# Kernel optimization log

Measured on AMD Instinct MI355X. Metric: run time of the kernel, lower is better.

## Reference

```python
import jax, jax.numpy as jnp
import numpy as np

B, N, C_IN = 8, 2048, 128
FEATS = [256, 256, 64]

def _mlp(x, W1, b1, W2, b2, W3, b3):
    # kernel-1 conv MLP == per-point linear layers; ReLU between hidden layers,
    # no ReLU on output (cfg mlp_with_relu=False)
    h = jax.nn.relu(jnp.einsum('bnc,fc->bnf', x, W1) + b1)
    h = jax.nn.relu(jnp.einsum('bnc,fc->bnf', h, W2) + b2)
    return jnp.einsum('bnc,fc->bnf', h, W3) + b3

def _pairwise_sqdist(u):
    # ||u_m - u_n||^2 expanded (avoids B*N*N*C intermediate)
    sq = jnp.sum(u * u, axis=-1)  # [B,N]
    d = sq[:, None, :] + sq[:, :, None] - 2.0 * jnp.einsum('bnc,bmc->bnm', u, u)
    return jnp.maximum(d, 0.0)

def setup_inputs() -> dict:
    key = jax.random.key(0)
    ks = jax.random.split(key, 8)
    x = jax.random.normal(ks[0], (B, N, C_IN), dtype=jnp.float32)
    labels = jax.random.randint(ks[1], (B, N), 0, 32, dtype=jnp.int32)
    tri = jax.random.randint(ks[2], (200, 3), 0, N, dtype=jnp.int32)
    W1 = jax.random.normal(ks[3], (FEATS[0], C_IN), dtype=jnp.float32) / np.sqrt(C_IN)
    b1 = jnp.zeros((FEATS[0],), jnp.float32)
    W2 = jax.random.normal(ks[4], (FEATS[1], FEATS[0]), dtype=jnp.float32) / np.sqrt(FEATS[0])
    b2 = jnp.zeros((FEATS[1],), jnp.float32)
    W3 = jax.random.normal(ks[5], (FEATS[2], FEATS[1]), dtype=jnp.float32) / np.sqrt(FEATS[1])
    b3 = jnp.zeros((FEATS[2],), jnp.float32)
    return {"x": x, "labels": labels, "tri": tri,
            "W1": W1, "b1": b1, "W2": W2, "b2": b2, "W3": W3, "b3": b3}

def _triplet_loss(dists, labels, tri):
    a, p, n = tri[:, 0], tri[:, 1], tri[:, 2]
    def per_batch(d, lab):
        valid = (a != p) & (lab[a] == lab[p]) & (lab[p] != lab[n])
        t = jnp.maximum(d[a, p] - d[a, n] + 2.0, 0.0)
        cnt = jnp.sum(valid)
        m = jnp.sum(jnp.where(valid, t, 0.0)) / jnp.maximum(cnt, 1).astype(t.dtype)
        use = (jnp.max(lab) > 0) & (cnt > 0)
        return jnp.where(use, m, 0.0)
    return jnp.sum(jax.vmap(per_batch)(dists, labels))

def _transitive_closure_clusters(dists):
    pred = (((dists + jnp.swapaxes(dists, 1, 2)) * 0.5) <= 1.0).astype(jnp.float32)
    idx = jnp.arange(N)
    pred = pred.at[:, idx, idx].set(1.0)
    def cond(s):
        _, now, before = s
        return now != before
    def body(s):
        m, now, _ = s
        m2 = (jnp.matmul(m, m) > 0).astype(jnp.float32)
        return (m2, jnp.sum(m2), now)
    s0 = (pred, jnp.sum(pred), jnp.sum(pred) - 1.0)
    pred, _, _ = jax.lax.while_loop(cond, body, s0)
    clusters = jnp.max(jnp.where(pred > 0, idx[None, :, None], -1), axis=1)
    return clusters.astype(jnp.int32)

def reference(x, labels, tri, W1, b1, W2, b2, W3, b3):
    u = _mlp(x, W1, b1, W2, b2, W3, b3)       # [B,N,C]
    dists = _pairwise_sqdist(u)               # [B,N,N]
    loss = _triplet_loss(dists, labels, tri)
    clusters = _transitive_closure_clusters(jax.lax.stop_gradient(dists))
    return (clusters, loss)
```

## Files before the change

### kernel.cpp

```cpp
#include <hip/hip_runtime.h>

constexpr int B_   = 8;
constexpr int N_   = 2048;
constexpr int CIN_ = 128;
constexpr int F1_  = 256;
constexpr int F2_  = 256;
constexpr int F3_  = 64;
constexpr int M_   = B_ * N_;

typedef unsigned short u16;
typedef unsigned long long u64;
typedef __attribute__((ext_vector_type(8)))  short short8v;
typedef __attribute__((ext_vector_type(16))) float f32x16;

__device__ inline u16 f2bf(float x){
    union { float f; unsigned u; } c; c.f = x;
    unsigned r = (c.u + 0x7FFFu + ((c.u >> 16) & 1u)) >> 16;
    return (u16)r;
}
__device__ inline float bf2f(u16 h){
    union { unsigned u; float f; } c; c.u = ((unsigned)h) << 16;
    return c.f;
}

constexpr int NX_  = M_ * CIN_;
constexpr int NW1_ = F1_ * CIN_;
constexpr int NW2_ = F2_ * F1_;

__global__ __launch_bounds__(256)
void split3_kernel(const float* __restrict__ x, const float* __restrict__ W1,
                   const float* __restrict__ W2,
                   u16* __restrict__ xh, u16* __restrict__ xm, u16* __restrict__ xl,
                   u16* __restrict__ w1h, u16* __restrict__ w1m, u16* __restrict__ w1l,
                   u16* __restrict__ w2h, u16* __restrict__ w2m, u16* __restrict__ w2l,
                   u64* __restrict__ rmask, float* __restrict__ lz)
{
    int id = blockIdx.x * 256 + threadIdx.x;
    if (id == 0) *lz = 0.f;
    if (id < M_) rmask[id] = 0ull;
    const float* src; u16 *oh, *om, *ol; int r, k, K;
    if (id < NX_)               { int t = id;               src = x;  r = t >> 7; k = t & 127; K = 128; oh = xh;  om = xm;  ol = xl;  }
    else if (id < NX_ + NW1_)   { int t = id - NX_;         src = W1; r = t >> 7; k = t & 127; K = 128; oh = w1h; om = w1m; ol = w1l; }
    else if (id < NX_ + NW1_ + NW2_) { int t = id - NX_ - NW1_; src = W2; r = t >> 8; k = t & 255; K = 256; oh = w2h; om = w2m; ol = w2l; }
    else return;
    float v = src[(size_t)r * K + k];
    u16 h = f2bf(v);            float vr = v - bf2f(h);
    u16 m = f2bf(vr);           u16 l = f2bf(vr - bf2f(m));
    size_t o = (size_t)r * K + (k ^ ((r & 7) << 3));
    oh[o] = h; om[o] = m; ol[o] = l;
}

template<int KSTEPS, int WRITE_F32>
__global__ __launch_bounds__(256)
void gemm_mfma(const u16* __restrict__ Ah, const u16* __restrict__ Am, const u16* __restrict__ Al,
               const u16* __restrict__ Wh, const u16* __restrict__ Wm, const u16* __restrict__ Wl,
               const float* __restrict__ bias,
               u16* __restrict__ Hh, u16* __restrict__ Hm, u16* __restrict__ Hl,
               float* __restrict__ Hf)
{
    constexpr int K = KSTEPS * 64;
    __shared__ __align__(16) u16 SMEM[3*64*64 + 3*128*64];
    u16* LA = SMEM;
    u16* LB = SMEM + 3*64*64;
    const int tid = threadIdx.x;
    const int wv = tid >> 6, l = tid & 63;
    const int wc = wv;
    const int lr = l & 31, hl = l >> 5;
    const int m0 = blockIdx.y * 64, f0 = blockIdx.x * 128;

    const u16* Asrc[3] = {Ah, Am, Al};
    const u16* Bsrc[3] = {Wh, Wm, Wl};

    f32x16 acc[2] = {};
    auto frag = [&](const u16* arr, int row, int kb) -> short8v {
        int off = row * 64 + ((kb ^ ((row & 7) << 4)) >> 1);
        return *(const short8v*)&arr[off];
    };

    for (int s = 0; s < KSTEPS; ++s) {
        const int k0 = s * 64;
        __syncthreads();
#pragma unroll
        for (int lvl = 0; lvl < 3; ++lvl) {
#pragma unroll
            for (int p = 0; p < 2; ++p) {
                int g = tid + p * 256;
                int row = g >> 3, ch = (g & 7) * 8;
                *(short8v*)&LA[lvl*4096 + row*64 + ch] =
                    *(const short8v*)&Asrc[lvl][(size_t)(m0 + row) * K + k0 + ch];
            }
#pragma unroll
            for (int p = 0; p < 4; ++p) {
                int g = tid + p * 256;
                int row = g >> 3, ch = (g & 7) * 8;
                *(short8v*)&LB[lvl*8192 + row*64 + ch] =
                    *(const short8v*)&Bsrc[lvl][(size_t)(f0 + row) * K + k0 + ch];
            }
        }
        __syncthreads();
#pragma unroll
        for (int ks = 0; ks < 4; ++ks) {
            const int kb = ks * 32 + hl * 16;
            short8v aF[3][2], bF[3];
#pragma unroll
            for (int lvl = 0; lvl < 3; ++lvl) {
#pragma unroll
                for (int ri = 0; ri < 2; ++ri)
                    aF[lvl][ri] = frag(LA + lvl*4096, ri*32 + lr, kb);
                bF[lvl] = frag(LB + lvl*8192, wc*32 + lr, kb);
            }
            const int pl[6][2] = {{0,2},{2,0},{1,1},{0,1},{1,0},{0,0}};
#pragma unroll
            for (int pp = 0; pp < 6; ++pp)
#pragma unroll
                for (int ri = 0; ri < 2; ++ri)
                    acc[ri] = __builtin_amdgcn_mfma_f32_32x32x16_bf16(
                        aF[pl[pp][0]][ri], bF[pl[pp][1]], acc[ri], 0, 0, 0);
        }
    }

    __syncthreads();
    float* LDSF = (float*)SMEM;
#pragma unroll
    for (int ri = 0; ri < 2; ++ri)
#pragma unroll
        for (int r = 0; r < 16; ++r) {
            int row = ri*32 + (r & 3) + 8*(r >> 2) + 4*hl;
            LDSF[row*132 + wc*32 + lr] = acc[ri][r];
        }
    __syncthreads();
#pragma unroll
    for (int p = 0; p < 4; ++p) {
        int idx = tid + p * 256;
        int row = idx >> 4;
        int g8  = (idx & 15) * 8;
        float v[8], bz[8];
        *(float4*)&v[0]  = *(const float4*)&LDSF[row*132 + g8];
        *(float4*)&v[4]  = *(const float4*)&LDSF[row*132 + g8 + 4];
        *(float4*)&bz[0] = *(const float4*)(bias + f0 + g8);
        *(float4*)&bz[4] = *(const float4*)(bias + f0 + g8 + 4);
        const size_t mrow = m0 + row;
        short8v hh, mm8, ll;
#pragma unroll
        for (int j = 0; j < 8; ++j) {
            float vv = fmaxf(v[j] + bz[j], 0.f);
            v[j] = vv;
            u16 h = f2bf(vv);  float r1 = vv - bf2f(h);
            u16 m = f2bf(r1);  u16 lo = f2bf(r1 - bf2f(m));
            hh[j] = (short)h; mm8[j] = (short)m; ll[j] = (short)lo;
        }
        if constexpr (WRITE_F32) {
            *(float4*)&Hf[mrow * F2_ + f0 + g8]     = *(const float4*)&v[0];
            *(float4*)&Hf[mrow * F2_ + f0 + g8 + 4] = *(const float4*)&v[4];
        }
        const size_t ob = mrow * F2_ + ((size_t)(f0 + g8) ^ ((mrow & 7) << 3));
        *(short8v*)&Hh[ob] = hh;
        *(short8v*)&Hm[ob] = mm8;
        *(short8v*)&Hl[ob] = ll;
    }
}

__global__ __launch_bounds__(256)
void gemm3_fused(const float* __restrict__ A, const float* __restrict__ W,
                 const float* __restrict__ bias, float* __restrict__ C,
                 u16* __restrict__ uh, u16* __restrict__ ul,
                 float* __restrict__ sqv)
{
    constexpr int K = 256;
    __shared__ __align__(16) float As[64][68];
    __shared__ __align__(16) float Ws[64][68];
    const int tid = threadIdx.x;
    const int tx = tid & 15, ty = tid >> 4;
    const int m0 = blockIdx.x * 64;

    float acc[4][4] = {};
    for (int k0 = 0; k0 < K; k0 += 64) {
        __syncthreads();
#pragma unroll
        for (int p = 0; p < 4; ++p) {
            int g = tid + p * 256;
            int r = g >> 4, c = (g & 15) << 2;
            float4 va = *(const float4*)(A + (size_t)(m0 + r) * K + k0 + c);
            As[c+0][r] = va.x; As[c+1][r] = va.y; As[c+2][r] = va.z; As[c+3][r] = va.w;
            float4 vw = *(const float4*)(W + (size_t)r * K + k0 + c);
            Ws[c+0][r] = vw.x; Ws[c+1][r] = vw.y; Ws[c+2][r] = vw.z; Ws[c+3][r] = vw.w;
        }
        __syncthreads();
#pragma unroll
        for (int k = 0; k < 64; ++k) {
            float a[4], w[4];
            *(float4*)&a[0] = *(const float4*)&As[k][ty << 2];
            *(float4*)&w[0] = *(const float4*)&Ws[k][tx << 2];
#pragma unroll
            for (int i = 0; i < 4; ++i)
#pragma unroll
                for (int j = 0; j < 4; ++j)
                    acc[i][j] = fmaf(a[i], w[j], acc[i][j]);
        }
    }

    float4 bz = *(const float4*)(bias + (tx << 2));
    const int slot = tx >> 1;
    const int hoff = (tx & 1) * 4;
#pragma unroll
    for (int i = 0; i < 4; ++i) {
        const int m = m0 + (ty << 2) + i;
        float o[4];
        o[0] = acc[i][0] + bz.x; o[1] = acc[i][1] + bz.y;
        o[2] = acc[i][2] + bz.z; o[3] = acc[i][3] + bz.w;
        *(float4*)(C + (size_t)m * F3_ + (tx << 2)) = *(const float4*)&o[0];
        ushort4 h4, l4;
        h4.x = f2bf(o[0]); l4.x = f2bf(o[0] - bf2f(h4.x));
        h4.y = f2bf(o[1]); l4.y = f2bf(o[1] - bf2f(h4.y));
        h4.z = f2bf(o[2]); l4.z = f2bf(o[2] - bf2f(h4.z));
        h4.w = f2bf(o[3]); l4.w = f2bf(o[3] - bf2f(h4.w));
        const int sb = (((slot * 16) ^ ((m & 7) << 4)) >> 1) + hoff;
        *(ushort4*)&uh[(size_t)m * 64 + sb] = h4;
        *(ushort4*)&ul[(size_t)m * 64 + sb] = l4;
        float s = o[0]*o[0] + o[1]*o[1] + o[2]*o[2] + o[3]*o[3];
#pragma unroll
        for (int msk = 1; msk <= 8; msk <<= 1) s += __shfl_xor(s, msk, 64);
        if (tx == 0) sqv[m] = s;
    }
}

__global__ __launch_bounds__(256)
void adj_mfma(const u16* __restrict__ uh, const u16* __restrict__ ul,
              const float* __restrict__ uf, const float* __restrict__ sqv,
              unsigned* __restrict__ adj, u64* __restrict__ rmask)
{
    __shared__ u16 UiH[128*64], UiL[128*64];
    __shared__ u16 UjH[128*64], UjL[128*64];
    __shared__ float sqi[128], sqj[128];
    const int tid = threadIdx.x;
    const int jt = blockIdx.x, it = blockIdx.y, b = blockIdx.z;
    const int i0 = it * 128, j0 = jt * 128;
    const size_t ub = (size_t)b * N_;

    if (tid < 128) sqi[tid] = sqv[ub + i0 + tid];
    else           sqj[tid - 128] = sqv[ub + j0 + (tid - 128)];

    auto stage = [&](const u16* src, u16* dst) {
#pragma unroll
        for (int p = 0; p < 4; ++p) {
            int g = tid + p * 256;
            *(short8v*)&dst[g * 8] = *(const short8v*)&src[g * 8];
        }
    };
    stage(uh + (ub + i0) * 64, UiH);
    stage(ul + (ub + i0) * 64, UiL);
    stage(uh + (ub + j0) * 64, UjH);
    stage(ul + (ub + j0) * 64, UjL);
    __syncthreads();

    const int w  = tid >> 6, l = tid & 63;
    const int wr = w >> 1,  wc = w & 1;
    const int lr = l & 31,  hl = l >> 5;

    f32x16 acc[2][2] = {};
    auto frag = [&](const u16* arr, int row, int kb) -> short8v {
        int off = row * 64 + ((kb ^ ((row & 7) << 4)) >> 1);
        return *(const short8v*)&arr[off];
    };
#pragma unroll
    for (int ks = 0; ks < 4; ++ks) {
        const int kb = ks * 32 + hl * 16;
        short8v aH[2], aL[2], bH[2], bL[2];
#pragma unroll
        for (int ri = 0; ri < 2; ++ri) {
            aH[ri] = frag(UiH, wr * 64 + ri * 32 + lr, kb);
            aL[ri] = frag(UiL, wr * 64 + ri * 32 + lr, kb);
        }
#pragma unroll
        for (int ci = 0; ci < 2; ++ci) {
            bH[ci] = frag(UjH, wc * 64 + ci * 32 + lr, kb);
            bL[ci] = frag(UjL, wc * 64 + ci * 32 + lr, kb);
        }
#pragma unroll
        for (int ri = 0; ri < 2; ++ri)
#pragma unroll
            for (int ci = 0; ci < 2; ++ci) {
                acc[ri][ci] = __builtin_amdgcn_mfma_f32_32x32x16_bf16(aH[ri], bH[ci], acc[ri][ci], 0, 0, 0);
                acc[ri][ci] = __builtin_amdgcn_mfma_f32_32x32x16_bf16(aH[ri], bL[ci], acc[ri][ci], 0, 0, 0);
                acc[ri][ci] = __builtin_amdgcn_mfma_f32_32x32x16_bf16(aL[ri], bH[ci], acc[ri][ci], 0, 0, 0);
            }
    }

#pragma unroll
    for (int ri = 0; ri < 2; ++ri)
#pragma unroll
    for (int ci = 0; ci < 2; ++ci) {
        const int Rb = wr * 64 + ri * 32;
        const int Cb = wc * 64 + ci * 32;
        const int jloc = Cb + lr;
        const float sj = sqj[jloc];
#pragma unroll
        for (int r = 0; r < 16; ++r) {
            const int base = (r & 3) + 8 * (r >> 2);
            const int iloc = Rb + base + 4 * hl;
            const float si = sqi[iloc];
            float dv = si + sj - 2.0f * acc[ri][ci][r];
            bool e;
            if (__builtin_expect(fabsf(dv - 1.0f) < 0.02f, 0)) {
                const float* ua = uf + (ub + i0 + iloc) * (size_t)F3_;
                const float* vb = uf + (ub + j0 + jloc) * (size_t)F3_;
                float dot = 0.f;
#pragma unroll 4
                for (int k = 0; k < F3_; ++k) dot = fmaf(ua[k], vb[k], dot);
                e = (si + sj - 2.0f * dot) <= 1.0f;
            } else {
                e = dv <= 1.0f;
            }
            u64 m = __ballot(e);
            if (l == 0) {
                const int I = i0 + Rb + base;
                const int W = (j0 + Cb) >> 5;
                adj[((size_t)b * 64 + W) * N_ + I]     = (unsigned)m;
                adj[((size_t)b * 64 + W) * N_ + I + 4] = (unsigned)(m >> 32);
                if ((unsigned)m)         atomicOr(&rmask[ub + I],     1ull << W);
                if ((unsigned)(m >> 32)) atomicOr(&rmask[ub + I + 4], 1ull << W);
            }
        }
    }
}

__global__ __launch_bounds__(1024)
void cc_kernel(const unsigned* __restrict__ adj, const u64* __restrict__ rmask,
               float* __restrict__ out)
{
    __shared__ int Lb[N_];
    __shared__ int chg;
    const int t = threadIdx.x;
    const int b = blockIdx.x;
    const unsigned* ab = adj + (size_t)b * 64 * N_;
    const u64* rm = rmask + (size_t)b * N_;

    Lb[t] = t; Lb[t + 1024] = t + 1024;
    __syncthreads();

    for (int iter = 0; iter < 24; ++iter) {
        if (t == 0) chg = 0;
        __syncthreads();
        int m[2], o[2];
#pragma unroll
        for (int h = 0; h < 2; ++h) {
            int i = t + h * 1024;
            int mm = Lb[i];
            o[h] = mm;
            const unsigned* row = ab + i;
            u64 msk = rm[i];
            while (msk) {
                int w = __ffsll(msk) - 1;
                msk &= msk - 1;
                unsigned v = row[(size_t)w * N_];
                while (v) {
                    int bit = __ffs(v) - 1;
                    v &= v - 1;
                    int lj = Lb[(w << 5) + bit];
                    mm = (lj > mm) ? lj : mm;
                }
            }
            for (int q = 0; q < N_; ++q) {
                int nx = Lb[mm];
                if (nx == mm) break;
                mm = nx;
            }
            m[h] = mm;
        }
        __syncthreads();
        Lb[t] = m[0]; Lb[t + 1024] = m[1];
        if (m[0] != o[0] || m[1] != o[1]) chg = 1;
        __syncthreads();
        if (!chg) break;
    }
    out[(size_t)b * N_ + t]        = (float)Lb[t];
    out[(size_t)b * N_ + t + 1024] = (float)Lb[t + 1024];
}

__global__ __launch_bounds__(256)
void sentinel_kernel(float* out, int n)
{
    int id = blockIdx.x * 256 + threadIdx.x;
    if (id < n) out[id] = -777.0f;
}

__global__ __launch_bounds__(256)
void loss_kernel(const float* __restrict__ u, const float* __restrict__ sq,
                 const int* __restrict__ labels, const int* __restrict__ tri,
                 float* __restrict__ loss)
{
    __shared__ float ssum[256];
    __shared__ int   scnt[256];
    __shared__ int   smax[256];
    const int b = blockIdx.x, t = threadIdx.x;
    const int base = b << 11;

    float mysum = 0.f; int mycnt = 0;
    if (t < 200) {
        int a = tri[3*t+0], p = tri[3*t+1], n = tri[3*t+2];
        int la = labels[base+a], lp = labels[base+p], ln = labels[base+n];
        bool valid = (a != p) && (la == lp) && (lp != ln);
        const float4* ua = (const float4*)(u + (size_t)(base + a) * F3_);
        const float4* up = (const float4*)(u + (size_t)(base + p) * F3_);
        const float4* un = (const float4*)(u + (size_t)(base + n) * F3_);
        float dap = 0.f, dan = 0.f;
#pragma unroll
        for (int q = 0; q < 16; ++q) {
            float4 va = ua[q], vp = up[q], vn = un[q];
            dap += va.x*vp.x + va.y*vp.y + va.z*vp.z + va.w*vp.w;
            dan += va.x*vn.x + va.y*vn.y + va.z*vn.z + va.w*vn.w;
        }
        float d1 = fmaxf(sq[base+a] + sq[base+p] - 2.f*dap, 0.f);
        float d2 = fmaxf(sq[base+a] + sq[base+n] - 2.f*dan, 0.f);
        float tt = fmaxf(d1 - d2 + 2.0f, 0.f);
        if (valid) { mysum = tt; mycnt = 1; }
    }
    int mymax = 0;
    for (int idx = t; idx < N_; idx += 256) {
        int lv = labels[base + idx];
        mymax = (lv > mymax) ? lv : mymax;
    }
    ssum[t] = mysum; scnt[t] = mycnt; smax[t] = mymax;
    __syncthreads();
    for (int s = 128; s > 0; s >>= 1) {
        if (t < s) {
            ssum[t] += ssum[t + s];
            scnt[t] += scnt[t + s];
            smax[t] = (smax[t + s] > smax[t]) ? smax[t + s] : smax[t];
        }
        __syncthreads();
    }
    if (t == 0) {
        int cnt = scnt[0];
        bool use = (smax[0] > 0) && (cnt > 0);
        float contrib = use ? (ssum[0] / (float)(cnt > 1 ? cnt : 1)) : 0.f;
        atomicAdd(loss, contrib);
    }
}

extern "C" void kernel_launch(void* const* d_in, const int* in_sizes, int n_in,
                              void* d_out, int out_size, void* d_ws, size_t ws_size,
                              hipStream_t stream)
{
    const float* x      = (const float*)d_in[0];
    const int*   labels = (const int*)  d_in[1];
    const int*   tri    = (const int*)  d_in[2];
    const float* W1     = (const float*)d_in[3];
    const float* b1     = (const float*)d_in[4];
    const float* W2     = (const float*)d_in[5];
    const float* b2     = (const float*)d_in[6];
    const float* W3     = (const float*)d_in[7];
    const float* b3     = (const float*)d_in[8];
    float* out = (float*)d_out;

    char* w = (char*)d_ws;
    size_t off = 0;
    auto carve = [&](size_t bytes) -> char* {
        char* p = w + off;
        off += (bytes + 255) & ~(size_t)255;
        return p;
    };
    u16* xh  = (u16*)carve((size_t)NX_  * 2);
    u16* xm  = (u16*)carve((size_t)NX_  * 2);
    u16* xl  = (u16*)carve((size_t)NX_  * 2);
    u16* w1h = (u16*)carve((size_t)NW1_ * 2);
    u16* w1m = (u16*)carve((size_t)NW1_ * 2);
    u16* w1l = (u16*)carve((size_t)NW1_ * 2);
    u16* w2h = (u16*)carve((size_t)NW2_ * 2);
    u16* w2m = (u16*)carve((size_t)NW2_ * 2);
    u16* w2l = (u16*)carve((size_t)NW2_ * 2);
    u16* h1h = (u16*)carve((size_t)M_ * F1_ * 2);
    u16* h1m = (u16*)carve((size_t)M_ * F1_ * 2);
    u16* h1l = (u16*)carve((size_t)M_ * F1_ * 2);
    u16* h2h = (u16*)carve((size_t)M_ * F2_ * 2);
    u16* h2m = (u16*)carve((size_t)M_ * F2_ * 2);
    u16* h2l = (u16*)carve((size_t)M_ * F2_ * 2);
    float* h2f = (float*)carve((size_t)M_ * F2_ * 4);
    float* u   = (float*)carve((size_t)M_ * F3_ * 4);
    u16*   uh  = (u16*)  carve((size_t)M_ * F3_ * 2);
    u16*   ul  = (u16*)  carve((size_t)M_ * F3_ * 2);
    float* sq  = (float*)carve((size_t)M_ * 4);
    unsigned* adj = (unsigned*)carve((size_t)B_ * 64 * N_ * 4);
    u64* rmask = (u64*)carve((size_t)M_ * 8);

    if (off > ws_size) {
        hipLaunchKernelGGL(sentinel_kernel, dim3((out_size + 255) / 256), dim3(256),
                           0, stream, out, out_size);
        return;
    }

    constexpr int NTOT = NX_ + NW1_ + NW2_;
    hipLaunchKernelGGL(split3_kernel, dim3((NTOT + 255) / 256), dim3(256), 0, stream,
                       x, W1, W2, xh, xm, xl, w1h, w1m, w1l, w2h, w2m, w2l,
                       rmask, out + M_);

    hipLaunchKernelGGL((gemm_mfma<2, 0>), dim3(F1_/128, M_/64), dim3(256), 0, stream,
                       xh, xm, xl, w1h, w1m, w1l, b1, h1h, h1m, h1l, (float*)nullptr);
    hipLaunchKernelGGL((gemm_mfma<4, 1>), dim3(F2_/128, M_/64), dim3(256), 0, stream,
                       h1h, h1m, h1l, w2h, w2m, w2l, b2, h2h, h2m, h2l, h2f);

    hipLaunchKernelGGL(gemm3_fused, dim3(M_/64), dim3(256), 0, stream,
                       h2f, W3, b3, u, uh, ul, sq);

    hipLaunchKernelGGL(adj_mfma, dim3(N_/128, N_/128, B_), dim3(256), 0, stream,
                       uh, ul, u, sq, adj, rmask);

    hipLaunchKernelGGL(loss_kernel, dim3(B_), dim3(256), 0, stream,
                       u, sq, labels, tri, out + M_);

    hipLaunchKernelGGL(cc_kernel, dim3(B_), dim3(1024), 0, stream,
                       adj, rmask, out);
}
```

Before: 183.6 us.

## Compute only upper-triangular adjacency tiles and mirror via bit transpose

```diff
diff --git a/kernel.cpp b/kernel.cpp
--- a/kernel.cpp
+++ b/kernel.cpp
@@ -167,32 +167,38 @@
                  float* __restrict__ sqv)
 {
     constexpr int K = 256;
-    __shared__ __align__(16) float As[64][68];
+    __shared__ __align__(16) float As[64][36];
     __shared__ __align__(16) float Ws[64][68];
     const int tid = threadIdx.x;
     const int tx = tid & 15, ty = tid >> 4;
-    const int m0 = blockIdx.x * 64;
-
-    float acc[4][4] = {};
+    const int m0 = blockIdx.x * 32;
+
+    float acc[2][4] = {};
     for (int k0 = 0; k0 < K; k0 += 64) {
         __syncthreads();
 #pragma unroll
-        for (int p = 0; p < 4; ++p) {
+        for (int p = 0; p < 2; ++p) {
             int g = tid + p * 256;
             int r = g >> 4, c = (g & 15) << 2;
             float4 va = *(const float4*)(A + (size_t)(m0 + r) * K + k0 + c);
             As[c+0][r] = va.x; As[c+1][r] = va.y; As[c+2][r] = va.z; As[c+3][r] = va.w;
+        }
+#pragma unroll
+        for (int p = 0; p < 4; ++p) {
+            int g = tid + p * 256;
+            int r = g >> 4, c = (g & 15) << 2;
             float4 vw = *(const float4*)(W + (size_t)r * K + k0 + c);
             Ws[c+0][r] = vw.x; Ws[c+1][r] = vw.y; Ws[c+2][r] = vw.z; Ws[c+3][r] = vw.w;
         }
         __syncthreads();
 #pragma unroll
         for (int k = 0; k < 64; ++k) {
-            float a[4], w[4];
-            *(float4*)&a[0] = *(const float4*)&As[k][ty << 2];
+            float a[2], w[4];
+            a[0] = As[k][(ty << 1)];
+            a[1] = As[k][(ty << 1) + 1];
             *(float4*)&w[0] = *(const float4*)&Ws[k][tx << 2];
 #pragma unroll
-            for (int i = 0; i < 4; ++i)
+            for (int i = 0; i < 2; ++i)
 #pragma unroll
                 for (int j = 0; j < 4; ++j)
                     acc[i][j] = fmaf(a[i], w[j], acc[i][j]);
@@ -203,8 +209,8 @@
     const int slot = tx >> 1;
     const int hoff = (tx & 1) * 4;
 #pragma unroll
-    for (int i = 0; i < 4; ++i) {
-        const int m = m0 + (ty << 2) + i;
+    for (int i = 0; i < 2; ++i) {
+        const int m = m0 + (ty << 1) + i;
         float o[4];
         o[0] = acc[i][0] + bz.x; o[1] = acc[i][1] + bz.y;
         o[2] = acc[i][2] + bz.z; o[3] = acc[i][3] + bz.w;
@@ -229,33 +235,35 @@
               const float* __restrict__ uf, const float* __restrict__ sqv,
               unsigned* __restrict__ adj, u64* __restrict__ rmask)
 {
-    __shared__ u16 UiH[128*64], UiL[128*64];
-    __shared__ u16 UjH[128*64], UjL[128*64];
+    __shared__ u16 UiH[128*64];
+    __shared__ u16 UjH[128*64];
     __shared__ float sqi[128], sqj[128];
     const int tid = threadIdx.x;
-    const int jt = blockIdx.x, it = blockIdx.y, b = blockIdx.z;
+    const int b = blockIdx.z;
+    int q = blockIdx.x;
+    int jt = (int)((sqrtf(8.f * q + 1.f) - 1.f) * 0.5f);
+    while ((jt + 1) * (jt + 2) / 2 <= q) ++jt;
+    while (jt * (jt + 1) / 2 > q) --jt;
+    const int it = q - jt * (jt + 1) / 2;
     const int i0 = it * 128, j0 = jt * 128;
     const size_t ub = (size_t)b * N_;
 
     if (tid < 128) sqi[tid] = sqv[ub + i0 + tid];
     else           sqj[tid - 128] = sqv[ub + j0 + (tid - 128)];
 
-    auto stage = [&](const u16* src, u16* dst) {
-#pragma unroll
-        for (int p = 0; p < 4; ++p) {
-            int g = tid + p * 256;
-            *(short8v*)&dst[g * 8] = *(const short8v*)&src[g * 8];
-        }
-    };
-    stage(uh + (ub + i0) * 64, UiH);
-    stage(ul + (ub + i0) * 64, UiL);
-    stage(uh + (ub + j0) * 64, UjH);
-    stage(ul + (ub + j0) * 64, UjL);
+#pragma unroll
+    for (int p = 0; p < 4; ++p) {
+        int g = tid + p * 256;
+        *(short8v*)&UiH[g * 8] = *(const short8v*)&uh[(ub + i0) * 64 + g * 8];
+        *(short8v*)&UjH[g * 8] = *(const short8v*)&uh[(ub + j0) * 64 + g * 8];
+    }
     __syncthreads();
 
     const int w  = tid >> 6, l = tid & 63;
     const int wr = w >> 1,  wc = w & 1;
     const int lr = l & 31,  hl = l >> 5;
+    const u16* ulI = ul + (ub + i0) * 64;
+    const u16* ulJ = ul + (ub + j0) * 64;
 
     f32x16 acc[2][2] = {};
     auto frag = [&](const u16* arr, int row, int kb) -> short8v {
@@ -269,12 +277,12 @@
 #pragma unroll
         for (int ri = 0; ri < 2; ++ri) {
             aH[ri] = frag(UiH, wr * 64 + ri * 32 + lr, kb);
-            aL[ri] = frag(UiL, wr * 64 + ri * 32 + lr, kb);
+            aL[ri] = frag(ulI, wr * 64 + ri * 32 + lr, kb);
         }
 #pragma unroll
         for (int ci = 0; ci < 2; ++ci) {
             bH[ci] = frag(UjH, wc * 64 + ci * 32 + lr, kb);
-            bL[ci] = frag(UjL, wc * 64 + ci * 32 + lr, kb);
+            bL[ci] = frag(ulJ, wc * 64 + ci * 32 + lr, kb);
         }
 #pragma unroll
         for (int ri = 0; ri < 2; ++ri)
@@ -320,6 +328,33 @@
                 if ((unsigned)m)         atomicOr(&rmask[ub + I],     1ull << W);
                 if ((unsigned)(m >> 32)) atomicOr(&rmask[ub + I + 4], 1ull << W);
             }
+        }
+    }
+}
+
+__global__ __launch_bounds__(256)
+void transpose_adj(unsigned* __restrict__ adj, u64* __restrict__ rmask)
+{
+    const int tid = threadIdx.x;
+    const int wv = tid >> 6, l = tid & 63;
+    const int bj = blockIdx.x * 4 + wv;
+    const int b  = blockIdx.y;
+    const int r  = l & 31, h = l >> 5;
+    unsigned* ab = adj + (size_t)b * 64 * N_;
+    for (int t = 0; t * 2 < bj; ++t) {
+        const int bi = t * 2 + h;
+        const bool act = bi < bj;
+        unsigned v = act ? ab[(size_t)bj * N_ + bi * 32 + r] : 0u;
+        unsigned wacc = 0u;
+#pragma unroll
+        for (int c = 0; c < 32; ++c) {
+            u64 m = __ballot((v >> c) & 1u);
+            if ((l & 31) == c) wacc = (h == 0) ? (unsigned)m : (unsigned)(m >> 32);
+        }
+        if (act) {
+            const int J = bj * 32 + (l & 31);
+            ab[(size_t)bi * N_ + J] = wacc;
+            if (wacc) atomicOr(&rmask[(size_t)b * N_ + J], 1ull << bi);
         }
     }
 }
@@ -499,11 +534,14 @@
     hipLaunchKernelGGL((gemm_mfma<4, 1>), dim3(F2_/128, M_/64), dim3(256), 0, stream,
                        h1h, h1m, h1l, w2h, w2m, w2l, b2, h2h, h2m, h2l, h2f);
 
-    hipLaunchKernelGGL(gemm3_fused, dim3(M_/64), dim3(256), 0, stream,
+    hipLaunchKernelGGL(gemm3_fused, dim3(M_/32), dim3(256), 0, stream,
                        h2f, W3, b3, u, uh, ul, sq);
 
-    hipLaunchKernelGGL(adj_mfma, dim3(N_/128, N_/128, B_), dim3(256), 0, stream,
+    hipLaunchKernelGGL(adj_mfma, dim3(136, 1, B_), dim3(256), 0, stream,
                        uh, ul, u, sq, adj, rmask);
+
+    hipLaunchKernelGGL(transpose_adj, dim3(16, B_), dim3(256), 0, stream,
+                       adj, rmask);
 
     hipLaunchKernelGGL(loss_kernel, dim3(B_), dim3(256), 0, stream,
                        u, sq, labels, tri, out + M_);
```

Result: slower. 198.6 us (+8.2%).
